# Kernel optimization log

Hardware: AMD Instinct MI355X
Metric: run time of the kernel (lower is better)

Reference implementation:

```python
import jax, jax.numpy as jnp
import numpy as np

N, E, IN, H, C = 50000, 800000, 256, 4, 32  # nodes, edges, in-dim, heads, per-head hidden
NEG_SLOPE = 0.2  # PyG GATConv default leaky_relu slope


def setup_inputs() -> dict:
    key = jax.random.key(0)
    ks = jax.random.split(key, 12)
    s = 0.05
    return {
        "x": jax.random.normal(ks[0], (N, IN), jnp.float32),
        "edge_index": jax.random.randint(ks[1], (2, E), 0, N),
        "root_index": jax.random.randint(ks[2], (1024,), 0, N),
        "W1": jax.random.normal(ks[3], (IN, H * C), jnp.float32) * s,
        "att_src1": jax.random.normal(ks[4], (H, C), jnp.float32) * s,
        "att_dst1": jax.random.normal(ks[5], (H, C), jnp.float32) * s,
        "b1": jnp.zeros((H * C,), jnp.float32),
        "W2": jax.random.normal(ks[6], (H * C, H * C), jnp.float32) * s,
        "att_src2": jax.random.normal(ks[7], (H, C), jnp.float32) * s,
        "att_dst2": jax.random.normal(ks[8], (H, C), jnp.float32) * s,
        "b2": jnp.zeros((H * C,), jnp.float32),
    }


def gat_conv(x, src, dst, W, a_src, a_dst, b, n_nodes, heads, out_c):
    # PyG GATConv (eval mode, concat=True, add_self_loops handled by caller).
    xp = (x @ W).reshape(n_nodes, heads, out_c)          # [N,H,C]
    alpha_s = jnp.sum(xp * a_src, axis=-1)               # [N,H]
    alpha_d = jnp.sum(xp * a_dst, axis=-1)               # [N,H]
    logits = jax.nn.leaky_relu(alpha_s[src] + alpha_d[dst], NEG_SLOPE)  # [Etot,H]
    # softmax over incoming edges per destination node
    lmax = jax.ops.segment_max(logits, dst, num_segments=n_nodes)
    ex = jnp.exp(logits - lmax[dst])
    denom = jax.ops.segment_sum(ex, dst, num_segments=n_nodes)
    alpha = ex / (denom[dst] + 1e-16)                    # [Etot,H]
    msg = xp[src] * alpha[:, :, None]                    # [Etot,H,C]
    out = jax.ops.segment_sum(msg, dst, num_segments=n_nodes)
    return out.reshape(n_nodes, heads * out_c) + b


def reference(x, edge_index, root_index, W1, att_src1, att_dst1, b1, W2, att_src2, att_dst2, b2):
    # add self loops once (PyG GATConv default add_self_loops=True)
    loop = jnp.arange(N, dtype=edge_index.dtype)
    src = jnp.concatenate([edge_index[0], loop])
    dst = jnp.concatenate([edge_index[1], loop])
    h = gat_conv(x, src, dst, W1, att_src1, att_dst1, b1, N, H, C)
    h = jax.nn.relu(h)
    h = gat_conv(h, src, dst, W2, att_src2, att_dst2, b2, N, H, C)
    return h[root_index].reshape(-1, h.shape[-1])
```

## Files before the change

### kernel.cpp

```cpp
#include <hip/hip_runtime.h>
#include <hip/hip_bf16.h>
#include <cstdint>
#include <cstddef>

constexpr int NN   = 50000;
constexpr int EE   = 800000;
constexpr int ETOT = EE + NN;
constexpr int HC   = 128;
constexpr float SLOPE = 0.2f;
constexpr int CAP  = 64;
constexpr int CSTR = 16;
constexpr int EBLOCKS = (ETOT + 255) / 256;
constexpr int GB      = (NN + 63) / 64;

typedef float f32x4  __attribute__((ext_vector_type(4)));
typedef short bf16x8 __attribute__((ext_vector_type(8)));


__device__ __forceinline__ ushort f2b(float f) {
  union { __hip_bfloat16 h; ushort u; } c;
  c.h = __float2bfloat16(f);
  return c.u;
}
__device__ __forceinline__ float b2f_lo(uint u) { return __uint_as_float(u << 16); }
__device__ __forceinline__ float b2f_hi(uint u) { return __uint_as_float(u & 0xffff0000u); }

union frag_cvt { uint4 u; bf16x8 b; };

__global__ __launch_bounds__(256)
void prep(const float* __restrict__ W1, const float* __restrict__ W2,
          const float* __restrict__ as1, const float* __restrict__ ad1,
          const float* __restrict__ b1,  const float* __restrict__ as2,
          const float* __restrict__ ad2, const float* __restrict__ b2,
          ushort* __restrict__ W1t, ushort* __restrict__ W2t,
          float* __restrict__ vecs, int* __restrict__ cnt,
          char* __restrict__ need, char* __restrict__ rflag) {
  const int tid = blockIdx.x * 256 + threadIdx.x;
  if (tid < NN) {
    cnt[tid * CSTR] = 0;
    need[tid] = 0;
    rflag[tid] = 0;
  }
  if (tid < 4096) {
    const int m = tid & 63, c = (tid >> 6) & 7, q = tid >> 9;
    const int kb = q * 32 + (m >> 4) * 8, n = c * 16 + (m & 15);
    #pragma unroll
    for (int j = 0; j < 8; ++j)
      W1t[tid * 8 + j] = f2b(W1[(size_t)(kb + j) * HC + n]);
  } else if (tid < 4096 + 2048) {
    const int t = tid - 4096;
    const int m = t & 63, c = (t >> 6) & 7, q = t >> 9;
    const int n = c * 16 + (m & 15);
    #pragma unroll
    for (int j = 0; j < 8; ++j) {
      const int p  = q * 32 + (m >> 4) * 8 + j;
      const int ko = (p >> 3) + ((p & 7) << 4);
      W2t[t * 8 + j] = f2b(W2[(size_t)ko * HC + n]);
    }
  } else if (tid < 4096 + 2048 + 768) {
    const int t = tid - 4096 - 2048;
    const int p = t & 127, which = t >> 7;
    const int c = (p >> 3) + ((p & 7) << 4);
    const float* src = which == 0 ? as1 : which == 1 ? ad1 : which == 2 ? b1
                     : which == 3 ? as2 : which == 4 ? ad2 : b2;
    vecs[which * 128 + p] = src[c];
  }
}

__global__ __launch_bounds__(256)
void mark_roots(const int* __restrict__ root, char* __restrict__ need,
                char* __restrict__ rflag, int n_root) {
  const int i = blockIdx.x * 256 + threadIdx.x;
  if (i < n_root) {
    const int r = root[i];
    rflag[r] = 1;
    need[r] = 1;
  }
}

__device__ __forceinline__ void edge_sd(const int* __restrict__ ei, int e,
                                        int& s, int& d) {
  if (e < EE) { s = ei[e]; d = ei[EE + e]; }
  else        { s = e - EE; d = s; }
}

__global__ __launch_bounds__(256)
void pass1(const int* __restrict__ ei, const char* __restrict__ rflag,
           char* __restrict__ need) {
  int e = blockIdx.x * 256 + threadIdx.x;
  if (e >= ETOT) return;
  int s, d; edge_sd(ei, e, s, d);
  if (rflag[d]) need[s] = 1;
}

__global__ __launch_bounds__(256)
void fillk(const int* __restrict__ ei, const char* __restrict__ need,
           int* __restrict__ cnt, ushort* __restrict__ slots) {
  int e = blockIdx.x * 256 + threadIdx.x;
  if (e >= ETOT) return;
  int s, d; edge_sd(ei, e, s, d);
  if (need[d]) {
    int pos = atomicAdd(cnt + d * CSTR, 1);
    if (pos < CAP) slots[((size_t)d << 6) + pos] = (ushort)s;
  }
}

template <int K>
__device__ __forceinline__
void gemm_body(int bid, const float* __restrict__ Xf,
               const ushort* __restrict__ Xb, const ushort* __restrict__ Wt,
               const float* __restrict__ attsp, const float* __restrict__ attdp,
               ushort* __restrict__ XPp, float* __restrict__ AS,
               float* __restrict__ AD) {
  const int l   = threadIdx.x & 63;
  const int wid = threadIdx.x >> 6;
  const int m0  = (bid * 4 + wid) * 16;
  const int lr  = l & 15, lg = l >> 4;
  const int arow = m0 + lr;
  const bool rowok = arow < NN;

  f32x4 acc[8];
  #pragma unroll
  for (int t = 0; t < 8; ++t) acc[t] = (f32x4)0.0f;

  for (int q = 0; q < K / 32; ++q) {
    frag_cvt a;
    if constexpr (K == 256) {
      float4 v0 = make_float4(0.f, 0.f, 0.f, 0.f), v1 = v0;
      if (rowok) {
        const float* p = Xf + (size_t)arow * K + q * 32 + lg * 8;
        v0 = *(const float4*)p;
        v1 = *(const float4*)(p + 4);
      }
      a.u.x = (uint)f2b(v0.x) | ((uint)f2b(v0.y) << 16);
      a.u.y = (uint)f2b(v0.z) | ((uint)f2b(v0.w) << 16);
      a.u.z = (uint)f2b(v1.x) | ((uint)f2b(v1.y) << 16);
      a.u.w = (uint)f2b(v1.z) | ((uint)f2b(v1.w) << 16);
    } else {
      a.u = rowok ? *(const uint4*)(Xb + (size_t)arow * K + q * 32 + lg * 8)
                  : make_uint4(0, 0, 0, 0);
    }
    const uint4* wq = (const uint4*)Wt + (size_t)(q * 8) * 64 + l;
    #pragma unroll
    for (int t = 0; t < 8; ++t) {
      frag_cvt b;
      b.u = wq[t * 64];
      acc[t] = __builtin_amdgcn_mfma_f32_16x16x32_bf16(a.b, b.b, acc[t],
                                                       0, 0, 0);
    }
  }

  float4 ap0 = *(const float4*)(attsp + lr * 8);
  float4 ap1 = *(const float4*)(attsp + lr * 8 + 4);
  float4 dp0 = *(const float4*)(attdp + lr * 8);
  float4 dp1 = *(const float4*)(attdp + lr * 8 + 4);
  const float av[8] = {ap0.x, ap0.y, ap0.z, ap0.w, ap1.x, ap1.y, ap1.z, ap1.w};
  const float dv[8] = {dp0.x, dp0.y, dp0.z, dp0.w, dp1.x, dp1.y, dp1.z, dp1.w};

  #pragma unroll
  for (int r = 0; r < 4; ++r) {
    const int orow = m0 + lg * 4 + r;
    const bool ok = orow < NN;
    if (ok) {
      uint4 pk;
      pk.x = (uint)f2b(acc[0][r]) | ((uint)f2b(acc[1][r]) << 16);
      pk.y = (uint)f2b(acc[2][r]) | ((uint)f2b(acc[3][r]) << 16);
      pk.z = (uint)f2b(acc[4][r]) | ((uint)f2b(acc[5][r]) << 16);
      pk.w = (uint)f2b(acc[6][r]) | ((uint)f2b(acc[7][r]) << 16);
      *(uint4*)(XPp + (size_t)orow * HC + lr * 8) = pk;
    }
    float s0 = acc[0][r] * av[0] + acc[1][r] * av[1];
    float s1 = acc[2][r] * av[2] + acc[3][r] * av[3];
    float s2 = acc[4][r] * av[4] + acc[5][r] * av[5];
    float s3 = acc[6][r] * av[6] + acc[7][r] * av[7];
    float d0 = acc[0][r] * dv[0] + acc[1][r] * dv[1];
    float d1 = acc[2][r] * dv[2] + acc[3][r] * dv[3];
    float d2 = acc[4][r] * dv[4] + acc[5][r] * dv[5];
    float d3 = acc[6][r] * dv[6] + acc[7][r] * dv[7];
    #pragma unroll
    for (int o = 1; o < 16; o <<= 1) {
      s0 += __shfl_xor(s0, o); s1 += __shfl_xor(s1, o);
      s2 += __shfl_xor(s2, o); s3 += __shfl_xor(s3, o);
      d0 += __shfl_xor(d0, o); d1 += __shfl_xor(d1, o);
      d2 += __shfl_xor(d2, o); d3 += __shfl_xor(d3, o);
    }
    if (lr == 0 && ok) {
      *(float4*)(AS + (size_t)orow * 4) = make_float4(s0, s1, s2, s3);
      *(float4*)(AD + (size_t)orow * 4) = make_float4(d0, d1, d2, d3);
    }
  }
}

__global__ __launch_bounds__(256)
void gemm1(const float* __restrict__ Xf, const ushort* __restrict__ Wt,
           const float* __restrict__ attsp, const float* __restrict__ attdp,
           ushort* __restrict__ XPp, float* __restrict__ AS,
           float* __restrict__ AD) {
  gemm_body<256>(blockIdx.x, Xf, nullptr, Wt, attsp, attdp, XPp, AS, AD);
}

__global__ __launch_bounds__(256)
void gemm2(const ushort* __restrict__ Xb, const ushort* __restrict__ Wt,
           const float* __restrict__ attsp, const float* __restrict__ attdp,
           ushort* __restrict__ XPp, float* __restrict__ AS,
           float* __restrict__ AD) {
  gemm_body<128>(blockIdx.x, nullptr, Xb, Wt, attsp, attdp, XPp, AS, AD);
}

__device__ __forceinline__ float wcalc(const float* AS, int s, int h, float adh) {
  float x = AS[(size_t)s * 4 + h] + adh;
  x = fmaxf(x, SLOPE * x);
  return __expf(x);
}

template <bool ROOT>
__global__ __launch_bounds__(256)
void aggregate(const int* __restrict__ roots, const char* __restrict__ need,
               const int* __restrict__ cnt, const ushort* __restrict__ slots,
               const float* __restrict__ AS, const float* __restrict__ AD,
               const uint* __restrict__ XPu, const float* __restrict__ bvp,
               void* __restrict__ outp) {
  const int nid = blockIdx.x * 4 + (threadIdx.x >> 6);
  const int node = ROOT ? roots[nid] : nid;
  if (!ROOT && !need[node]) return;
  const int l = threadIdx.x & 63;
  const int h = l & 3;
  const int deg = min(cnt[node * CSTR], CAP);
  const size_t base = (size_t)node << 6;
  const float adh = AD[((size_t)node << 2) + h];
  const int si = (int)slots[base + l];

  float ax = 0.f, ay = 0.f, den = 0.f;
  int e = 0;
  for (; e + 4 <= deg; e += 4) {
    const int s0 = __shfl(si, e),     s1 = __shfl(si, e + 1);
    const int s2 = __shfl(si, e + 2), s3 = __shfl(si, e + 3);
    const uint u0 = XPu[((size_t)s0 << 6) + l];
    const uint u1 = XPu[((size_t)s1 << 6) + l];
    const uint u2 = XPu[((size_t)s2 << 6) + l];
    const uint u3 = XPu[((size_t)s3 << 6) + l];
    const float w0 = wcalc(AS, s0, h, adh), w1 = wcalc(AS, s1, h, adh);
    const float w2 = wcalc(AS, s2, h, adh), w3 = wcalc(AS, s3, h, adh);
    ax += w0 * b2f_lo(u0) + w1 * b2f_lo(u1) + w2 * b2f_lo(u2) + w3 * b2f_lo(u3);
    ay += w0 * b2f_hi(u0) + w1 * b2f_hi(u1) + w2 * b2f_hi(u2) + w3 * b2f_hi(u3);
    den += (w0 + w1) + (w2 + w3);
  }
  for (; e < deg; ++e) {
    const int s = __shfl(si, e);
    const uint u = XPu[((size_t)s << 6) + l];
    const float w = wcalc(AS, s, h, adh);
    ax += w * b2f_lo(u);
    ay += w * b2f_hi(u);
    den += w;
  }

  const float inv = 1.f / (den + 1e-16f);
  const float2 bv = *(const float2*)(bvp + 2 * l);
  float rx = ax * inv + bv.x;
  float ry = ay * inv + bv.y;
  if (ROOT) {
    const int col0 = 32 * (l & 3) + (l >> 2);
    float* o = (float*)outp + (size_t)nid * HC;
    o[col0] = rx;
    o[col0 + 16] = ry;
  } else {
    rx = fmaxf(rx, 0.f);
    ry = fmaxf(ry, 0.f);
    ((uint*)outp)[((size_t)node << 6) + l] = (uint)f2b(rx) | ((uint)f2b(ry) << 16);
  }
}

extern "C" void kernel_launch(void* const* d_in, const int* in_sizes, int n_in,
                              void* d_out, int out_size, void* d_ws, size_t ws_size,
                              hipStream_t stream) {
  const float* x    = (const float*)d_in[0];
  const int*   ei   = (const int*)d_in[1];
  const int*   root = (const int*)d_in[2];
  const float* W1   = (const float*)d_in[3];
  const float* as1  = (const float*)d_in[4];
  const float* ad1  = (const float*)d_in[5];
  const float* b1   = (const float*)d_in[6];
  const float* W2   = (const float*)d_in[7];
  const float* as2  = (const float*)d_in[8];
  const float* ad2  = (const float*)d_in[9];
  const float* b2   = (const float*)d_in[10];
  float* out = (float*)d_out;

  ushort* W1t  = (ushort*)d_ws;
  ushort* W2t  = W1t + 4096 * 8;
  float*  vecs = (float*)(W2t + 2048 * 8);
  ushort* XPp  = (ushort*)(vecs + 768);
  ushort* Hbp  = XPp + (size_t)NN * HC;
  float*  AS   = (float*)(Hbp + (size_t)NN * HC);
  float*  AD   = AS + (size_t)NN * 4;
  int*    cnt  = (int*)(AD + (size_t)NN * 4);
  ushort* slots = (ushort*)(cnt + (size_t)NN * CSTR);
  char*   need  = (char*)(slots + (size_t)NN * CAP);
  char*   rflag = need + NN;

  const int n_root = out_size / HC;

  prep<<<224, 256, 0, stream>>>(W1, W2, as1, ad1, b1, as2, ad2, b2,
                                W1t, W2t, vecs, cnt, need, rflag);
  mark_roots<<<(n_root + 255) / 256, 256, 0, stream>>>(root, need, rflag,
                                                       n_root);
  pass1<<<EBLOCKS, 256, 0, stream>>>(ei, rflag, need);
  fillk<<<EBLOCKS, 256, 0, stream>>>(ei, need, cnt, slots);

  gemm1<<<GB, 256, 0, stream>>>(x, W1t, vecs, vecs + 128, XPp, AS, AD);
  aggregate<false><<<NN / 4, 256, 0, stream>>>(nullptr, need, cnt, slots,
                                               AS, AD, (const uint*)XPp,
                                               vecs + 256, Hbp);

  gemm2<<<GB, 256, 0, stream>>>(Hbp, W2t, vecs + 384, vecs + 512,
                                XPp, AS, AD);
  aggregate<true><<<n_root / 4, 256, 0, stream>>>(root, need, cnt, slots,
                                                  AS, AD, (const uint*)XPp,
                                                  vecs + 640, out);
}
```

Measured before the change: 188.0 us.

## Compact needed-node list, fuse fill into gemm1, compact gemm2 rows

Builds a compact list of needed nodes with atomics, replacing the need-flag scan. Layer-1 aggregation and the layer-2 GEMM now run only over listed nodes instead of all nodes with early exits. The slot-fill pass is merged into the layer-1 GEMM launch as extra blocks, saving a launch and letting the two overlap. The aggregation inner loop is unrolled to 8 loads in flight. The costs are extra atomics, node order in the list that is not deterministic, and indirect row gathers in the GEMM.

```diff
diff --git a/kernel.cpp b/kernel.cpp
--- a/kernel.cpp
+++ b/kernel.cpp
@@ -10,7 +10,8 @@
 constexpr float SLOPE = 0.2f;
 constexpr int CAP  = 64;
 constexpr int CSTR = 16;
-constexpr int EBLOCKS = (ETOT + 255) / 256;
+constexpr int EB_ALL  = (ETOT + 255) / 256;
+constexpr int EB_EDGE = (EE + 255) / 256;
 constexpr int GB      = (NN + 63) / 64;
 
 typedef float f32x4  __attribute__((ext_vector_type(4)));
@@ -34,8 +35,10 @@
           const float* __restrict__ ad2, const float* __restrict__ b2,
           ushort* __restrict__ W1t, ushort* __restrict__ W2t,
           float* __restrict__ vecs, int* __restrict__ cnt,
-          char* __restrict__ need, char* __restrict__ rflag) {
+          int* __restrict__ need, char* __restrict__ rflag,
+          int* __restrict__ n1cnt) {
   const int tid = blockIdx.x * 256 + threadIdx.x;
+  if (tid == 0) *n1cnt = 0;
   if (tid < NN) {
     cnt[tid * CSTR] = 0;
     need[tid] = 0;
@@ -68,56 +71,55 @@
 }
 
 __global__ __launch_bounds__(256)
-void mark_roots(const int* __restrict__ root, char* __restrict__ need,
-                char* __restrict__ rflag, int n_root) {
+void mark_roots(const int* __restrict__ root, int* __restrict__ need,
+                char* __restrict__ rflag, int* __restrict__ n1cnt,
+                int* __restrict__ list, int n_root) {
   const int i = blockIdx.x * 256 + threadIdx.x;
-  if (i < n_root) {
-    const int r = root[i];
-    rflag[r] = 1;
-    need[r] = 1;
-  }
-}
-
-__device__ __forceinline__ void edge_sd(const int* __restrict__ ei, int e,
-                                        int& s, int& d) {
-  if (e < EE) { s = ei[e]; d = ei[EE + e]; }
-  else        { s = e - EE; d = s; }
+  if (i >= n_root) return;
+  const int r = root[i];
+  rflag[r] = 1;
+  if (atomicOr(need + r, 1) == 0) {
+    list[atomicAdd(n1cnt, 1)] = r;
+  }
 }
 
 __global__ __launch_bounds__(256)
 void pass1(const int* __restrict__ ei, const char* __restrict__ rflag,
-           char* __restrict__ need) {
-  int e = blockIdx.x * 256 + threadIdx.x;
-  if (e >= ETOT) return;
-  int s, d; edge_sd(ei, e, s, d);
-  if (rflag[d]) need[s] = 1;
-}
-
-__global__ __launch_bounds__(256)
-void fillk(const int* __restrict__ ei, const char* __restrict__ need,
-           int* __restrict__ cnt, ushort* __restrict__ slots) {
-  int e = blockIdx.x * 256 + threadIdx.x;
-  if (e >= ETOT) return;
-  int s, d; edge_sd(ei, e, s, d);
-  if (need[d]) {
-    int pos = atomicAdd(cnt + d * CSTR, 1);
-    if (pos < CAP) slots[((size_t)d << 6) + pos] = (ushort)s;
-  }
-}
-
-template <int K>
+           int* __restrict__ need, int* __restrict__ n1cnt,
+           int* __restrict__ list) {
+  const int e = blockIdx.x * 256 + threadIdx.x;
+  if (e >= EE) return;
+  const int d = ei[EE + e];
+  if (rflag[d]) {
+    const int s = ei[e];
+    if (need[s] == 0 && atomicOr(need + s, 1) == 0)
+      list[atomicAdd(n1cnt, 1)] = s;
+  }
+}
+
+template <int K, bool COMPACT>
 __device__ __forceinline__
 void gemm_body(int bid, const float* __restrict__ Xf,
                const ushort* __restrict__ Xb, const ushort* __restrict__ Wt,
                const float* __restrict__ attsp, const float* __restrict__ attdp,
                ushort* __restrict__ XPp, float* __restrict__ AS,
-               float* __restrict__ AD) {
+               float* __restrict__ AD, const int* __restrict__ list,
+               const int* __restrict__ nlim) {
   const int l   = threadIdx.x & 63;
   const int wid = threadIdx.x >> 6;
   const int m0  = (bid * 4 + wid) * 16;
   const int lr  = l & 15, lg = l >> 4;
-  const int arow = m0 + lr;
-  const bool rowok = arow < NN;
+
+  int lim = NN, arow;
+  if constexpr (COMPACT) {
+    lim = *nlim;
+    if (m0 >= lim) return;
+    const int aidx = m0 + lr;
+    arow = (aidx < lim) ? list[aidx] : -1;
+  } else {
+    arow = m0 + lr;
+  }
+  const bool rowok = COMPACT ? (arow >= 0) : (arow < NN);
 
   f32x4 acc[8];
   #pragma unroll
@@ -159,8 +161,14 @@
 
   #pragma unroll
   for (int r = 0; r < 4; ++r) {
-    const int orow = m0 + lg * 4 + r;
-    const bool ok = orow < NN;
+    int orow; bool ok;
+    if constexpr (COMPACT) {
+      ok = (m0 + lg * 4 + r) < lim;
+      orow = __shfl(arow, lg * 4 + r);
+    } else {
+      orow = m0 + lg * 4 + r;
+      ok = orow < NN;
+    }
     if (ok) {
       uint4 pk;
       pk.x = (uint)f2b(acc[0][r]) | ((uint)f2b(acc[1][r]) << 16);
@@ -191,20 +199,41 @@
   }
 }
 
-__global__ __launch_bounds__(256)
-void gemm1(const float* __restrict__ Xf, const ushort* __restrict__ Wt,
-           const float* __restrict__ attsp, const float* __restrict__ attdp,
-           ushort* __restrict__ XPp, float* __restrict__ AS,
-           float* __restrict__ AD) {
-  gemm_body<256>(blockIdx.x, Xf, nullptr, Wt, attsp, attdp, XPp, AS, AD);
+__device__ __forceinline__ void edge_sd(const int* __restrict__ ei, int e,
+                                        int& s, int& d) {
+  if (e < EE) { s = ei[e]; d = ei[EE + e]; }
+  else        { s = e - EE; d = s; }
+}
+
+__global__ __launch_bounds__(256)
+void gemm1_fill(const float* __restrict__ Xf, const ushort* __restrict__ Wt,
+                const float* __restrict__ attsp, const float* __restrict__ attdp,
+                ushort* __restrict__ XPp, float* __restrict__ AS,
+                float* __restrict__ AD, const int* __restrict__ ei,
+                const int* __restrict__ need, int* __restrict__ cnt,
+                ushort* __restrict__ slots) {
+  if (blockIdx.x < GB) {
+    gemm_body<256, false>(blockIdx.x, Xf, nullptr, Wt, attsp, attdp,
+                          XPp, AS, AD, nullptr, nullptr);
+  } else {
+    const int e = (blockIdx.x - GB) * 256 + threadIdx.x;
+    if (e >= ETOT) return;
+    int s, d; edge_sd(ei, e, s, d);
+    if (need[d]) {
+      const int pos = atomicAdd(cnt + d * CSTR, 1);
+      if (pos < CAP) slots[((size_t)d << 6) + pos] = (ushort)s;
+    }
+  }
 }
 
 __global__ __launch_bounds__(256)
 void gemm2(const ushort* __restrict__ Xb, const ushort* __restrict__ Wt,
            const float* __restrict__ attsp, const float* __restrict__ attdp,
            ushort* __restrict__ XPp, float* __restrict__ AS,
-           float* __restrict__ AD) {
-  gemm_body<128>(blockIdx.x, nullptr, Xb, Wt, attsp, attdp, XPp, AS, AD);
+           float* __restrict__ AD, const int* __restrict__ list,
+           const int* __restrict__ nlim) {
+  gemm_body<128, true>(blockIdx.x, nullptr, Xb, Wt, attsp, attdp,
+                       XPp, AS, AD, list, nlim);
 }
 
 __device__ __forceinline__ float wcalc(const float* AS, int s, int h, float adh) {
@@ -215,14 +244,14 @@
 
 template <bool ROOT>
 __global__ __launch_bounds__(256)
-void aggregate(const int* __restrict__ roots, const char* __restrict__ need,
+void aggregate(const int* __restrict__ idx, const int* __restrict__ nlim,
                const int* __restrict__ cnt, const ushort* __restrict__ slots,
                const float* __restrict__ AS, const float* __restrict__ AD,
                const uint* __restrict__ XPu, const float* __restrict__ bvp,
                void* __restrict__ outp) {
   const int nid = blockIdx.x * 4 + (threadIdx.x >> 6);
-  const int node = ROOT ? roots[nid] : nid;
-  if (!ROOT && !need[node]) return;
+  if (!ROOT && nid >= *nlim) return;
+  const int node = idx[nid];
   const int l = threadIdx.x & 63;
   const int h = l & 3;
   const int deg = min(cnt[node * CSTR], CAP);
@@ -232,18 +261,20 @@
 
   float ax = 0.f, ay = 0.f, den = 0.f;
   int e = 0;
-  for (; e + 4 <= deg; e += 4) {
-    const int s0 = __shfl(si, e),     s1 = __shfl(si, e + 1);
-    const int s2 = __shfl(si, e + 2), s3 = __shfl(si, e + 3);
-    const uint u0 = XPu[((size_t)s0 << 6) + l];
-    const uint u1 = XPu[((size_t)s1 << 6) + l];
-    const uint u2 = XPu[((size_t)s2 << 6) + l];
-    const uint u3 = XPu[((size_t)s3 << 6) + l];
-    const float w0 = wcalc(AS, s0, h, adh), w1 = wcalc(AS, s1, h, adh);
-    const float w2 = wcalc(AS, s2, h, adh), w3 = wcalc(AS, s3, h, adh);
-    ax += w0 * b2f_lo(u0) + w1 * b2f_lo(u1) + w2 * b2f_lo(u2) + w3 * b2f_lo(u3);
-    ay += w0 * b2f_hi(u0) + w1 * b2f_hi(u1) + w2 * b2f_hi(u2) + w3 * b2f_hi(u3);
-    den += (w0 + w1) + (w2 + w3);
+  for (; e + 8 <= deg; e += 8) {
+    int ss[8]; uint uu[8]; float wv[8];
+    #pragma unroll
+    for (int j = 0; j < 8; ++j) ss[j] = __shfl(si, e + j);
+    #pragma unroll
+    for (int j = 0; j < 8; ++j) uu[j] = XPu[((size_t)ss[j] << 6) + l];
+    #pragma unroll
+    for (int j = 0; j < 8; ++j) wv[j] = wcalc(AS, ss[j], h, adh);
+    #pragma unroll
+    for (int j = 0; j < 8; ++j) {
+      ax += wv[j] * b2f_lo(uu[j]);
+      ay += wv[j] * b2f_hi(uu[j]);
+      den += wv[j];
+    }
   }
   for (; e < deg; ++e) {
     const int s = __shfl(si, e);
@@ -295,26 +326,29 @@
   float*  AD   = AS + (size_t)NN * 4;
   int*    cnt  = (int*)(AD + (size_t)NN * 4);
   ushort* slots = (ushort*)(cnt + (size_t)NN * CSTR);
-  char*   need  = (char*)(slots + (size_t)NN * CAP);
-  char*   rflag = need + NN;
+  int*    need  = (int*)(slots + (size_t)NN * CAP);
+  int*    list  = need + NN;
+  int*    n1cnt = list + NN;
+  char*   rflag = (char*)(n1cnt + 4);
 
   const int n_root = out_size / HC;
 
   prep<<<224, 256, 0, stream>>>(W1, W2, as1, ad1, b1, as2, ad2, b2,
-                                W1t, W2t, vecs, cnt, need, rflag);
+                                W1t, W2t, vecs, cnt, need, rflag, n1cnt);
   mark_roots<<<(n_root + 255) / 256, 256, 0, stream>>>(root, need, rflag,
-                                                       n_root);
-  pass1<<<EBLOCKS, 256, 0, stream>>>(ei, rflag, need);
-  fillk<<<EBLOCKS, 256, 0, stream>>>(ei, need, cnt, slots);
-
-  gemm1<<<GB, 256, 0, stream>>>(x, W1t, vecs, vecs + 128, XPp, AS, AD);
-  aggregate<false><<<NN / 4, 256, 0, stream>>>(nullptr, need, cnt, slots,
-                                               AS, AD, (const uint*)XPp,
-                                               vecs + 256, Hbp);
+                                                       n1cnt, list, n_root);
+  pass1<<<EB_EDGE, 256, 0, stream>>>(ei, rflag, need, n1cnt, list);
+
+  gemm1_fill<<<GB + EB_ALL, 256, 0, stream>>>(x, W1t, vecs, vecs + 128,
+                                              XPp, AS, AD,
+                                              ei, need, cnt, slots);
+  aggregate<false><<<(NN + 3) / 4, 256, 0, stream>>>(list, n1cnt, cnt, slots,
+                                                     AS, AD, (const uint*)XPp,
+                                                     vecs + 256, Hbp);
 
   gemm2<<<GB, 256, 0, stream>>>(Hbp, W2t, vecs + 384, vecs + 512,
-                                XPp, AS, AD);
-  aggregate<true><<<n_root / 4, 256, 0, stream>>>(root, need, cnt, slots,
+                                XPp, AS, AD, list, n1cnt);
+  aggregate<true><<<n_root / 4, 256, 0, stream>>>(root, nullptr, cnt, slots,
                                                   AS, AD, (const uint*)XPp,
                                                   vecs + 640, out);
 }
```

Result: slower. 289.5 us (+54.0%).
